# Kernel optimization log

Measured on AMD Instinct MI355X. Metric: run time of the kernel, lower is better.

The kernel has to match this reference:

```python
import jax, jax.numpy as jnp
import numpy as np

BATCH_SIZE = 4096
TEMPERATURE = 0.5
DIAG_NEG = -50000.0
EPS = 1e-8  # torch CosineSimilarity eps


def setup_inputs() -> dict:
    key = jax.random.key(0)
    k1, k2 = jax.random.split(key)
    z_i = jax.random.normal(k1, (BATCH_SIZE, 128), dtype=jnp.float32)
    z_j = jax.random.normal(k2, (BATCH_SIZE, 128), dtype=jnp.float32)
    return {"z_i": z_i, "z_j": z_j}


def reference(z_i, z_j):
    n = z_i.shape[0]
    z = jnp.concatenate([z_i, z_j], axis=0)  # [2N, D]
    # cosine similarity: normalize once, then one GEMM (same math as
    # CosineSimilarity(dim=2) on the broadcasted pair, with eps clamp on norms)
    norms = jnp.maximum(jnp.linalg.norm(z, axis=-1, keepdims=True), EPS)
    zn = z / norms
    sim = (zn @ zn.T) / TEMPERATURE  # [2N, 2N]
    # mask self-similarity on the diagonal
    idx = jnp.arange(2 * n)
    sim = sim.at[idx, idx].set(DIAG_NEG)
    # labels: positive pair is the other view
    labels = jnp.concatenate([idx[n:], idx[:n]])  # [2N]
    # mean softmax cross-entropy
    logp = jax.nn.log_softmax(sim, axis=-1)
    loss = -jnp.mean(logp[idx, labels])
    return loss
```

## Files before the change

kernel.cpp:

```cpp
#include <hip/hip_runtime.h>

#define N2 8192
#define NHALF 4096
#define DDIM 128
#define NCHUNK 16
#define CPC 512
#define NT 8
#define RPB 512
#define LN2F 0.69314718055994530942f
#define SCALEF 1.6986436f

typedef __attribute__((ext_vector_type(8))) short bf8_t;
typedef __attribute__((ext_vector_type(4))) float f4_t;

__device__ __forceinline__ float fexp2(float x) { return __builtin_amdgcn_exp2f(x); }
__device__ __forceinline__ float flog2(float x) { return __builtin_amdgcn_logf(x); }

__device__ __forceinline__ unsigned short f2bf(float f) {
  unsigned int x = __float_as_uint(f);
  x += 0x7fffu + ((x >> 16) & 1u);
  return (unsigned short)(x >> 16);
}
__device__ __forceinline__ float bf2f(unsigned short h) {
  return __uint_as_float(((unsigned int)h) << 16);
}

__global__ __launch_bounds__(256) void knorm(const float* __restrict__ zi,
                                             const float* __restrict__ zj,
                                             unsigned short* __restrict__ u,
                                             float* __restrict__ dhat) {
  const int lane = threadIdx.x & 63;
  const int row = blockIdx.x * 4 + (threadIdx.x >> 6);
  const float* src = (row < NHALF) ? (zi + (size_t)row * DDIM)
                                   : (zj + (size_t)(row - NHALF) * DDIM);
  float2 x = *(const float2*)(src + lane * 2);
  float ss = x.x * x.x + x.y * x.y;
#pragma unroll
  for (int m = 32; m; m >>= 1) ss += __shfl_xor(ss, m);
  float scale = SCALEF / fmaxf(sqrtf(ss), 1e-8f);
  unsigned short b0 = f2bf(x.x * scale);
  unsigned short b1 = f2bf(x.y * scale);
  *(unsigned int*)(u + (size_t)row * DDIM + lane * 2) =
      (unsigned int)b0 | ((unsigned int)b1 << 16);
  float f0 = bf2f(b0), f1 = bf2f(b1);
  float dd = f0 * f0 + f1 * f1;
#pragma unroll
  for (int m = 32; m; m >>= 1) dd += __shfl_xor(dd, m);
  if (lane == 0) dhat[row] = dd;
}

__global__ __launch_bounds__(1024) void ksim(const unsigned short* __restrict__ u,
                                             float* __restrict__ Lp) {
  __shared__ short Bls[24576];
  const int tid = threadIdx.x;
  const int lane = tid & 63;
  const int w = tid >> 6;
  const int rb = blockIdx.x >> 4;
  const int chunk = blockIdx.x & 15;
  const int lr = lane & 15, lq = lane >> 4;
  const int rowbase = rb * RPB + w * 32;
  const int colbase = chunk * CPC;

  bf8_t a[2][4];
#pragma unroll
  for (int s = 0; s < 2; s++)
#pragma unroll
    for (int kc = 0; kc < 4; kc++)
      a[s][kc] = *(const bf8_t*)(u + (size_t)(rowbase + s * 16 + lr) * DDIM +
                                 kc * 32 + lq * 8);
#pragma unroll
  for (int s = 0; s < 2; s++)
#pragma unroll
    for (int kc = 0; kc < 4; kc++)
      asm volatile("" : "+v"(a[s][kc]));

  f4_t L0 = {0.f, 0.f, 0.f, 0.f}, L1 = {0.f, 0.f, 0.f, 0.f};

  auto STAGE = [&](int t) {
    const int col_local = w * 4 + lq;
    const int sdu = lr ^ (4 * (w & 1) + lq);
    const unsigned short* src =
        u + (size_t)(colbase + t * 64 + col_local) * DDIM + sdu * 8;
    short* dst = &Bls[(t % 3) * 8192 + w * 512];
    __builtin_amdgcn_global_load_lds(
        (const __attribute__((address_space(1))) unsigned int*)src,
        (__attribute__((address_space(3))) unsigned int*)dst, 16, 0, 0);
  };

  auto COMP = [&](int t) {
    const short* P = &Bls[(t % 3) * 8192];
#pragma unroll
    for (int g = 0; g < 4; g++) {
      bf8_t bv[4];
#pragma unroll
      for (int kc = 0; kc < 4; kc++)
        bv[kc] = *(const bf8_t*)&P[((g * 16 + lr) * 16 +
                                    ((kc * 4 + lq) ^ (lr & 7))) * 8];
      f4_t acc0 = {0.f, 0.f, 0.f, 0.f}, acc1 = {0.f, 0.f, 0.f, 0.f};
#pragma unroll
      for (int kc = 0; kc < 4; kc++) {
        acc0 = __builtin_amdgcn_mfma_f32_16x16x32_bf16(a[0][kc], bv[kc], acc0, 0, 0, 0);
        acc1 = __builtin_amdgcn_mfma_f32_16x16x32_bf16(a[1][kc], bv[kc], acc1, 0, 0, 0);
      }
#pragma unroll
      for (int r = 0; r < 4; r++) {
        L0[r] += fexp2(acc0[r]);
        L1[r] += fexp2(acc1[r]);
      }
    }
  };

  STAGE(0);
  STAGE(1);
#pragma unroll 1
  for (int t = 0; t < NT; ++t) {
    if (t < NT - 1) {
      asm volatile("s_waitcnt vmcnt(1)" ::: "memory");
    } else {
      asm volatile("s_waitcnt vmcnt(0)" ::: "memory");
    }
    __builtin_amdgcn_sched_barrier(0);
    __builtin_amdgcn_s_barrier();
    __builtin_amdgcn_sched_barrier(0);
    COMP(t);
    if (t + 2 < NT) STAGE(t + 2);
  }

#pragma unroll
  for (int r = 0; r < 4; r++) {
    float v0 = L0[r], v1 = L1[r];
    v0 += __shfl_xor(v0, 1); v0 += __shfl_xor(v0, 2);
    v0 += __shfl_xor(v0, 4); v0 += __shfl_xor(v0, 8);
    v1 += __shfl_xor(v1, 1); v1 += __shfl_xor(v1, 2);
    v1 += __shfl_xor(v1, 4); v1 += __shfl_xor(v1, 8);
    if (lr == 0) {
      const int rrow = rowbase + lq * 4 + r;
      Lp[(size_t)rrow * NCHUNK + chunk] = v0;
      Lp[(size_t)(rrow + 16) * NCHUNK + chunk] = v1;
    }
  }
}

__global__ __launch_bounds__(256) void krow(const unsigned short* __restrict__ u,
                                            const float* __restrict__ dhat,
                                            const float* __restrict__ Lp,
                                            float* __restrict__ bsum) {
  const int lane = threadIdx.x & 63;
  const int w = threadIdx.x >> 6;
  const int i = blockIdx.x * 4 + w;
  const int j = (i + NHALF) & (N2 - 1);

  const unsigned int av = ((const unsigned int*)(u + (size_t)i * DDIM))[lane];
  const unsigned int bv = ((const unsigned int*)(u + (size_t)j * DDIM))[lane];
  float dot = __uint_as_float(av << 16) * __uint_as_float(bv << 16) +
              __uint_as_float(av & 0xffff0000u) * __uint_as_float(bv & 0xffff0000u);
  float ls = (lane < NCHUNK) ? Lp[(size_t)i * NCHUNK + lane] : 0.f;
#pragma unroll
  for (int m = 32; m; m >>= 1) {
    dot += __shfl_xor(dot, m);
    ls += __shfl_xor(ls, m);
  }
  __shared__ float sred[4];
  if (lane == 0) {
    const float L = ls - fexp2(dhat[i]);
    sred[w] = LN2F * (flog2(L) - dot);
  }
  __syncthreads();
  if (threadIdx.x == 0)
    bsum[blockIdx.x] = sred[0] + sred[1] + sred[2] + sred[3];
}

__global__ void kfinal(const float* __restrict__ bsum, float* __restrict__ out) {
  float v = 0.f;
#pragma unroll
  for (int jj = 0; jj < 32; jj++) v += bsum[threadIdx.x + 64 * jj];
#pragma unroll
  for (int m = 32; m; m >>= 1) v += __shfl_xor(v, m);
  if (threadIdx.x == 0) out[0] = v * (1.0f / N2);
}

extern "C" void kernel_launch(void* const* d_in, const int* in_sizes, int n_in,
                              void* d_out, int out_size, void* d_ws, size_t ws_size,
                              hipStream_t stream) {
  const float* zi = (const float*)d_in[0];
  const float* zj = (const float*)d_in[1];
  char* ws = (char*)d_ws;
  unsigned short* u = (unsigned short*)ws;
  float* dhat = (float*)(ws + (size_t)N2 * DDIM * 2);
  float* Lp = (float*)(ws + (size_t)N2 * DDIM * 2 + (size_t)N2 * 4);
  float* bsum = (float*)(ws + (size_t)N2 * DDIM * 2 + (size_t)N2 * 4 +
                         (size_t)NCHUNK * N2 * 4);
  float* out = (float*)d_out;

  hipLaunchKernelGGL(knorm, dim3(N2 / 4), dim3(256), 0, stream, zi, zj, u, dhat);
  hipLaunchKernelGGL(ksim, dim3((N2 / RPB) * NCHUNK), dim3(1024), 0, stream, u, Lp);
  hipLaunchKernelGGL(krow, dim3(N2 / 4), dim3(256), 0, stream, u, dhat, Lp, bsum);
  hipLaunchKernelGGL(kfinal, dim3(1), dim3(64), 0, stream, bsum, out);
}
```

Measured before the change: 36.31 us.

## Exploit symmetry of similarity matrix by computing only upper-triangular tiles

Because the similarity matrix is symmetric, the sim kernel now launches blocks only for upper-triangular 256x256 tiles. Each off-diagonal tile contributes row sums for its row block and also column sums, reduced through shared memory, for the transposed block. This roughly halves the MFMA and exp work. In exchange it adds shuffles, a shared-memory reduction, a triangular index decode loop, smaller 512-thread blocks, and a wider partial-sum buffer for the row kernel to read.

```diff
diff --git a/kernel.cpp b/kernel.cpp
--- a/kernel.cpp
+++ b/kernel.cpp
@@ -3,10 +3,9 @@
 #define N2 8192
 #define NHALF 4096
 #define DDIM 128
-#define NCHUNK 16
-#define CPC 512
-#define NT 8
-#define RPB 512
+#define NB 32
+#define NSLOT 32
+#define NT 4
 #define LN2F 0.69314718055994530942f
 #define SCALEF 1.6986436f
 
@@ -49,17 +48,20 @@
   if (lane == 0) dhat[row] = dd;
 }
 
-__global__ __launch_bounds__(1024) void ksim(const unsigned short* __restrict__ u,
-                                             float* __restrict__ Lp) {
+__global__ __launch_bounds__(512) void ksim(const unsigned short* __restrict__ u,
+                                            float* __restrict__ Lp) {
   __shared__ short Bls[24576];
+  __shared__ float CSl[8][256];
   const int tid = threadIdx.x;
   const int lane = tid & 63;
   const int w = tid >> 6;
-  const int rb = blockIdx.x >> 4;
-  const int chunk = blockIdx.x & 15;
+  int bres = blockIdx.x, I = 0;
+  while (bres >= NB - I) { bres -= NB - I; I++; }
+  const int J = I + bres;
+  const bool offdiag = (J > I);
   const int lr = lane & 15, lq = lane >> 4;
-  const int rowbase = rb * RPB + w * 32;
-  const int colbase = chunk * CPC;
+  const int rowbase = I * 256 + w * 32;
+  const int colbase = J * 256;
 
   bf8_t a[2][4];
 #pragma unroll
@@ -77,14 +79,18 @@
   f4_t L0 = {0.f, 0.f, 0.f, 0.f}, L1 = {0.f, 0.f, 0.f, 0.f};
 
   auto STAGE = [&](int t) {
-    const int col_local = w * 4 + lq;
-    const int sdu = lr ^ (4 * (w & 1) + lq);
-    const unsigned short* src =
-        u + (size_t)(colbase + t * 64 + col_local) * DDIM + sdu * 8;
-    short* dst = &Bls[(t % 3) * 8192 + w * 512];
-    __builtin_amdgcn_global_load_lds(
-        (const __attribute__((address_space(1))) unsigned int*)src,
-        (__attribute__((address_space(3))) unsigned int*)dst, 16, 0, 0);
+#pragma unroll
+    for (int i = 0; i < 2; i++) {
+      const int j = w * 2 + i;
+      const int col_local = j * 4 + lq;
+      const int sdu = lr ^ (4 * (j & 1) + lq);
+      const unsigned short* src =
+          u + (size_t)(colbase + t * 64 + col_local) * DDIM + sdu * 8;
+      short* dst = &Bls[(t % 3) * 8192 + j * 512];
+      __builtin_amdgcn_global_load_lds(
+          (const __attribute__((address_space(1))) unsigned int*)src,
+          (__attribute__((address_space(3))) unsigned int*)dst, 16, 0, 0);
+    }
   };
 
   auto COMP = [&](int t) {
@@ -102,10 +108,18 @@
         acc0 = __builtin_amdgcn_mfma_f32_16x16x32_bf16(a[0][kc], bv[kc], acc0, 0, 0, 0);
         acc1 = __builtin_amdgcn_mfma_f32_16x16x32_bf16(a[1][kc], bv[kc], acc1, 0, 0, 0);
       }
+      float s8 = 0.f;
 #pragma unroll
       for (int r = 0; r < 4; r++) {
-        L0[r] += fexp2(acc0[r]);
-        L1[r] += fexp2(acc1[r]);
+        const float e0 = fexp2(acc0[r]);
+        const float e1 = fexp2(acc1[r]);
+        L0[r] += e0; L1[r] += e1;
+        s8 += e0 + e1;
+      }
+      if (offdiag) {
+        s8 += __shfl_xor(s8, 16);
+        s8 += __shfl_xor(s8, 32);
+        if (lq == 0) CSl[w][t * 64 + g * 16 + lr] = s8;
       }
     }
   };
@@ -115,7 +129,7 @@
 #pragma unroll 1
   for (int t = 0; t < NT; ++t) {
     if (t < NT - 1) {
-      asm volatile("s_waitcnt vmcnt(1)" ::: "memory");
+      asm volatile("s_waitcnt vmcnt(2)" ::: "memory");
     } else {
       asm volatile("s_waitcnt vmcnt(0)" ::: "memory");
     }
@@ -135,8 +149,17 @@
     v1 += __shfl_xor(v1, 4); v1 += __shfl_xor(v1, 8);
     if (lr == 0) {
       const int rrow = rowbase + lq * 4 + r;
-      Lp[(size_t)rrow * NCHUNK + chunk] = v0;
-      Lp[(size_t)(rrow + 16) * NCHUNK + chunk] = v1;
+      Lp[(size_t)rrow * NSLOT + J] = v0;
+      Lp[(size_t)(rrow + 16) * NSLOT + J] = v1;
+    }
+  }
+  if (offdiag) {
+    __syncthreads();
+    if (tid < 256) {
+      float cs = 0.f;
+#pragma unroll
+      for (int k = 0; k < 8; k++) cs += CSl[k][tid];
+      Lp[(size_t)(colbase + tid) * NSLOT + I] = cs;
     }
   }
 }
@@ -154,7 +177,7 @@
   const unsigned int bv = ((const unsigned int*)(u + (size_t)j * DDIM))[lane];
   float dot = __uint_as_float(av << 16) * __uint_as_float(bv << 16) +
               __uint_as_float(av & 0xffff0000u) * __uint_as_float(bv & 0xffff0000u);
-  float ls = (lane < NCHUNK) ? Lp[(size_t)i * NCHUNK + lane] : 0.f;
+  float ls = (lane < NSLOT) ? Lp[(size_t)i * NSLOT + lane] : 0.f;
 #pragma unroll
   for (int m = 32; m; m >>= 1) {
     dot += __shfl_xor(dot, m);
@@ -189,11 +212,11 @@
   float* dhat = (float*)(ws + (size_t)N2 * DDIM * 2);
   float* Lp = (float*)(ws + (size_t)N2 * DDIM * 2 + (size_t)N2 * 4);
   float* bsum = (float*)(ws + (size_t)N2 * DDIM * 2 + (size_t)N2 * 4 +
-                         (size_t)NCHUNK * N2 * 4);
+                         (size_t)NSLOT * N2 * 4);
   float* out = (float*)d_out;
 
   hipLaunchKernelGGL(knorm, dim3(N2 / 4), dim3(256), 0, stream, zi, zj, u, dhat);
-  hipLaunchKernelGGL(ksim, dim3((N2 / RPB) * NCHUNK), dim3(1024), 0, stream, u, Lp);
+  hipLaunchKernelGGL(ksim, dim3(NB * (NB + 1) / 2), dim3(512), 0, stream, u, Lp);
   hipLaunchKernelGGL(krow, dim3(N2 / 4), dim3(256), 0, stream, u, dhat, Lp, bsum);
   hipLaunchKernelGGL(kfinal, dim3(1), dim3(64), 0, stream, bsum, out);
 }
```

After: 37.82 us. 1.04x slower.
